# Kernel optimization log

Measured on AMD Instinct MI355X. Metric: run time of the kernel, lower is better.

The kernel has to match this reference:

```python
import jax, jax.numpy as jnp
import numpy as np

B, T, C = 8, 2048, 1024  # micro_bsz, seq_len, n_embd (== complexsize)


def setup_inputs() -> dict:
    key = jax.random.key(0)
    ks = jax.random.split(key, 6)
    w = lambda k, shape: (jax.random.normal(k, shape, dtype=jnp.float32) * 0.02)
    return {
        "x": jax.random.normal(ks[0], (B, T, C), dtype=jnp.float32),
        "Wk": w(ks[1], (2 * C, C)),      # key: n_embd -> 2*n_embd (no bias)
        "Wa": w(ks[2], (C, 2 * C)),      # activation: 2*n_embd -> n_embd (no bias)
        "Wf": w(ks[3], (2, C, C)),       # WaveNet filter conv, kernel=2, WIO layout
        "Wg": w(ks[4], (2, C, C)),       # WaveNet gate conv, kernel=2, WIO layout
        "Wo": w(ks[5], (C, C)),          # WaveNet 1x1 output projection
    }


def _causal_conv(x, W):
    # x: [B,T,Cin], W: [K,Cin,Cout]; left-pad K-1 for causality
    return jax.lax.conv_general_dilated(
        x, W, window_strides=(1,), padding=[(W.shape[0] - 1, 0)],
        dimension_numbers=("NWC", "WIO", "NWC"))


def _wavenet_short(x, Wf, Wg, Wo):
    # undialated gated WaveNet unit: tanh(conv_f(x)) * sigmoid(conv_g(x)) -> 1x1 proj
    h = jnp.tanh(_causal_conv(x, Wf)) * jax.nn.sigmoid(_causal_conv(x, Wg))
    return h @ Wo.T


def reference(x, Wk, Wa, Wf, Wg, Wo):
    Bx, Tx, Cx = x.shape
    k = (x @ Wk.T).reshape(Bx, Tx, Cx, 2)                 # [B,T,C,2]
    cv = jax.lax.complex(k[..., 0], k[..., 1])            # view_as_complex -> [B,T,C]
    scale = jax.lax.cummax(jnp.abs(cv), axis=1)           # running max of magnitude
    cv2 = cv / scale.astype(cv.dtype)                      # normalize magnitude <= 1
    kv = jnp.cumprod(cv2, axis=1)                          # complex cumulative product
    re = jnp.stack([kv.real, kv.imag], axis=-1).reshape(Bx, Tx, 2 * Cx)  # view_as_real
    return (re @ Wa.T) * _wavenet_short(x * scale, Wf, Wg, Wo)
```

## Files before the change

kernel.cpp:

```cpp
#include <hip/hip_runtime.h>
#include <cmath>

#define T_SEQ 2048
#define C_DIM 1024
#define BM 128
#define BN 128
#define BK 32

typedef unsigned short u16;
typedef unsigned int u32;
typedef short bf16x8 __attribute__((ext_vector_type(8)));
typedef _Float16 f16x8 __attribute__((ext_vector_type(8)));
typedef float f32x4 __attribute__((ext_vector_type(4)));
typedef unsigned short u16x8 __attribute__((ext_vector_type(8)));

#define AS1 __attribute__((address_space(1)))
#define AS3 __attribute__((address_space(3)))

__device__ __forceinline__ u16 f2bf(float f) {
    u32 u = __builtin_bit_cast(u32, f);
    u32 r = u + 0x7fffu + ((u >> 16) & 1u);
    return (u16)(r >> 16);
}
__device__ __forceinline__ u16 f2h(float f) {
    return __builtin_bit_cast(u16, (_Float16)f);
}
__device__ __forceinline__ float h2f(u16 h) {
    return (float)__builtin_bit_cast(_Float16, h);
}
__device__ __forceinline__ void gl_lds16(const void* g, void* l) {
    __builtin_amdgcn_global_load_lds((const AS1 u32*)g, (AS3 u32*)l, 16, 0, 0);
}

__device__ __forceinline__ int xcd_swz(int lin, int nwg) {
    return (lin & 7) * (nwg >> 3) + (lin >> 3);
}

#define SBAR() do { __builtin_amdgcn_sched_barrier(0); \
                    __builtin_amdgcn_s_barrier(); \
                    __builtin_amdgcn_sched_barrier(0); } while (0)
#define VMC(n) do { asm volatile("s_waitcnt vmcnt(" #n ")" ::: "memory"); \
                    __builtin_amdgcn_sched_barrier(0); } while (0)

__global__ __launch_bounds__(512, 2)
void gemm8(const u16* __restrict__ Ap, const u16* __restrict__ Bp,
           u16* __restrict__ Cout, int M, int N, int K)
{
    __shared__ u16 lds[2 * 32768];
    const int tid  = threadIdx.x;
    const int lane = tid & 63;
    const int wid  = tid >> 6;
    const int wrow = wid >> 2;
    const int wcol = wid & 3;
    const int gx = gridDim.x;
    const int lin = xcd_swz(blockIdx.x + gx * blockIdx.y, gx * gridDim.y);
    const int m0 = (lin / gx) * 256;
    const int n0 = (lin % gx) * 256;
    const int NT = K / 64;

    f32x4 acc[8][4] = {};

    auto stageu = [&](int t, int u) {
        const int isB = u & 1, kh = u >> 1;
        u16* ubase = &lds[(t & 1) * 32768 + isB * 16384 + kh * 8192];
        const u16* src = isB ? Bp + (size_t)n0 * K : Ap + (size_t)m0 * K;
        const int k0 = t * 64 + kh * 32;
        #pragma unroll
        for (int j = 0; j < 2; ++j) {
            const int c = wid + 8 * j;
            const int p = c * 64 + lane;
            const int row = p >> 2;
            const int sp  = (p & 3) ^ ((row >> 1) & 3);
            gl_lds16(src + (size_t)row * K + k0 + sp * 8, ubase + c * 512);
        }
    };

    auto lda = [&](int buf, int kh, int mq, f16x8 (&a)[4]) {
        const u16* base = &lds[buf * 32768 + kh * 8192];
        #pragma unroll
        for (int f = 0; f < 4; ++f) {
            const int row = wrow * 128 + mq * 64 + f * 16 + (lane & 15);
            const int sp  = (lane >> 4) ^ ((row >> 1) & 3);
            a[f] = *(const f16x8*)&base[row * 32 + sp * 8];
        }
    };
    auto ldb = [&](int buf, int kh, f16x8 (&b)[4]) {
        const u16* base = &lds[buf * 32768 + 16384 + kh * 8192];
        #pragma unroll
        for (int f = 0; f < 4; ++f) {
            const int row = wcol * 64 + f * 16 + (lane & 15);
            const int sp  = (lane >> 4) ^ ((row >> 1) & 3);
            b[f] = *(const f16x8*)&base[row * 32 + sp * 8];
        }
    };
    auto mm = [&](const f16x8 (&a)[4], const f16x8 (&b)[4], int mq) {
        __builtin_amdgcn_s_setprio(1);
        #pragma unroll
        for (int fm = 0; fm < 4; ++fm)
            #pragma unroll
            for (int fn = 0; fn < 4; ++fn)
                acc[mq * 4 + fm][fn] = __builtin_amdgcn_mfma_f32_16x16x32_f16(
                    a[fm], b[fn], acc[mq * 4 + fm][fn], 0, 0, 0);
        __builtin_amdgcn_s_setprio(0);
    };

    stageu(0, 0); stageu(0, 1); stageu(0, 2); stageu(0, 3);
    VMC(4);
    SBAR();

    f16x8 a[4], b[4];
    for (int t = 0; t < NT; ++t) {
        const int buf = t & 1;
        const bool more = (t + 1 < NT);
        if (more) { stageu(t + 1, 0); VMC(6); } else { VMC(4); }
        lda(buf, 0, 0, a); ldb(buf, 0, b);
        mm(a, b, 0);
        SBAR();
        if (more) stageu(t + 1, 1);
        lda(buf, 0, 1, a);
        mm(a, b, 1);
        SBAR();
        if (more) { stageu(t + 1, 2); VMC(6); } else { VMC(0); }
        lda(buf, 1, 0, a); ldb(buf, 1, b);
        mm(a, b, 0);
        SBAR();
        if (more) stageu(t + 1, 3);
        lda(buf, 1, 1, a);
        mm(a, b, 1);
        SBAR();
    }

    const int crow0 = m0 + wrow * 128 + ((lane >> 4) << 2);
    const int ccol  = n0 + wcol * 64 + (lane & 15);
    #pragma unroll
    for (int mi = 0; mi < 8; ++mi)
        #pragma unroll
        for (int fn = 0; fn < 4; ++fn)
            #pragma unroll
            for (int r = 0; r < 4; ++r)
                Cout[(size_t)(crow0 + mi * 16 + r) * N + ccol + fn * 16] =
                    f2h(acc[mi][fn][r]);
}

__global__ __launch_bounds__(256)
void dual_gemm(const u16* __restrict__ A1, const u16* __restrict__ B1, int K1,
               const u16* __restrict__ A2, const u16* __restrict__ B2, int K2,
               float* __restrict__ out, int M, int N)
{
    __shared__ u16 lds[2 * 2 * 4096];
    const int tid  = threadIdx.x;
    const int lane = tid & 63;
    const int wid  = tid >> 6;
    const int wr = wid >> 1, wc = wid & 1;
    const int gx = gridDim.x;
    const int lin = xcd_swz(blockIdx.x + gx * blockIdx.y, gx * gridDim.y);
    const int m0 = (lin / gx) * BM;
    const int n0 = (lin % gx) * BN;

    f32x4 acc1[4][4] = {};
    f32x4 acc2[4][4] = {};

    auto stage = [&](const u16* Ap, const u16* Bp, int K, int it, int buf) {
        const int k0 = it * BK;
        u16* base = &lds[buf * 8192];
        #pragma unroll
        for (int i = 0; i < 2; ++i) {
            const int chunk = wid + 4 * i;
            const int rloc  = chunk * 16 + (lane >> 2);
            const int slot  = (lane & 3) ^ ((rloc >> 1) & 3);
            gl_lds16(Bp + (size_t)(n0 + rloc) * K + k0 + slot * 8,
                     base + 4096 + chunk * 512);
            gl_lds16(Ap + (size_t)(m0 + rloc) * K + k0 + slot * 8,
                     base + chunk * 512);
        }
    };

    auto compute = [&](int buf, f32x4 (&acc)[4][4]) {
        const u16* base = &lds[buf * 8192];
        bf16x8 a[4], b[4];
        #pragma unroll
        for (int f = 0; f < 4; ++f) {
            const int row = wr * 64 + f * 16 + (lane & 15);
            const int sp  = ((lane >> 4) & 3) ^ ((row >> 1) & 3);
            a[f] = *(const bf16x8*)&base[row * 32 + sp * 8];
            const int rowb = wc * 64 + f * 16 + (lane & 15);
            const int spb  = ((lane >> 4) & 3) ^ ((rowb >> 1) & 3);
            b[f] = *(const bf16x8*)&base[4096 + rowb * 32 + spb * 8];
        }
        #pragma unroll
        for (int fm = 0; fm < 4; ++fm)
            #pragma unroll
            for (int fn = 0; fn < 4; ++fn)
                acc[fm][fn] = __builtin_amdgcn_mfma_f32_16x16x32_bf16(a[fm], b[fn], acc[fm][fn], 0, 0, 0);
    };

    const int NT1 = K1 / BK, NT2 = K2 / BK;
    stage(A1, B1, K1, 0, 0);
    int cur = 0;
    for (int it = 0; it < NT1; ++it) {
        __syncthreads();
        if (it + 1 < NT1) stage(A1, B1, K1, it + 1, cur ^ 1);
        else              stage(A2, B2, K2, 0, cur ^ 1);
        compute(cur, acc1);
        cur ^= 1;
    }
    for (int it = 0; it < NT2; ++it) {
        __syncthreads();
        if (it + 1 < NT2) stage(A2, B2, K2, it + 1, cur ^ 1);
        compute(cur, acc2);
        cur ^= 1;
    }

    const int crow0 = m0 + wr * 64 + ((lane >> 4) << 2);
    const int ccol  = n0 + wc * 64 + (lane & 15);
    #pragma unroll
    for (int fm = 0; fm < 4; ++fm)
        #pragma unroll
        for (int fn = 0; fn < 4; ++fn)
            #pragma unroll
            for (int r = 0; r < 4; ++r) {
                const size_t idx = (size_t)(crow0 + fm * 16 + r) * N + ccol + fn * 16;
                out[idx] = acc1[fm][fn][r] * acc2[fm][fn][r];
            }
}

__global__ __launch_bounds__(256)
void conv_gate(const u16* __restrict__ A, const u16* __restrict__ Wfgt,
               u16* __restrict__ H, int M)
{
    constexpr int KIT = C_DIM / BK;
    constexpr int NT  = 2 * KIT;
    __shared__ u16 lds[2 * 3 * 4096];
    const int tid  = threadIdx.x;
    const int lane = tid & 63;
    const int wid  = tid >> 6;
    const int wr = wid >> 1, wc = wid & 1;
    const int gx = gridDim.x;
    const int lin = xcd_swz(blockIdx.x + gx * blockIdx.y, gx * gridDim.y);
    const int m0 = (lin / gx) * BM;
    const int n0 = (lin % gx) * BN;

    f32x4 accF[4][4] = {};
    f32x4 accG[4][4] = {};

    auto stage = [&](int it, int buf) {
        const int p  = it / KIT;
        const int k0 = (it - p * KIT) * BK;
        u16* base = &lds[buf * 12288];
        const u16* BF = Wfgt + (size_t)p * 2 * C_DIM * C_DIM;
        const u16* BG = BF + (size_t)C_DIM * C_DIM;
        const int sh = (p == 0) ? 1 : 0;
        #pragma unroll
        for (int i = 0; i < 2; ++i) {
            const int chunk = wid + 4 * i;
            const int rloc  = chunk * 16 + (lane >> 2);
            const int slot  = (lane & 3) ^ ((rloc >> 1) & 3);
            int grow = m0 + rloc - sh;
            if (grow < 0) grow = 0;
            gl_lds16(A + (size_t)grow * C_DIM + k0 + slot * 8,
                     base + chunk * 512);
            gl_lds16(BF + (size_t)(n0 + rloc) * C_DIM + k0 + slot * 8,
                     base + 4096 + chunk * 512);
            gl_lds16(BG + (size_t)(n0 + rloc) * C_DIM + k0 + slot * 8,
                     base + 8192 + chunk * 512);
        }
    };

    auto compute = [&](int buf) {
        const u16* base = &lds[buf * 12288];
        bf16x8 a[4], bf[4], bg[4];
        #pragma unroll
        for (int f = 0; f < 4; ++f) {
            const int row = wr * 64 + f * 16 + (lane & 15);
            const int sp  = ((lane >> 4) & 3) ^ ((row >> 1) & 3);
            a[f] = *(const bf16x8*)&base[row * 32 + sp * 8];
            const int rowb = wc * 64 + f * 16 + (lane & 15);
            const int spb  = ((lane >> 4) & 3) ^ ((rowb >> 1) & 3);
            bf[f] = *(const bf16x8*)&base[4096 + rowb * 32 + spb * 8];
            bg[f] = *(const bf16x8*)&base[8192 + rowb * 32 + spb * 8];
        }
        #pragma unroll
        for (int fm = 0; fm < 4; ++fm)
            #pragma unroll
            for (int fn = 0; fn < 4; ++fn) {
                accF[fm][fn] = __builtin_amdgcn_mfma_f32_16x16x32_bf16(a[fm], bf[fn], accF[fm][fn], 0, 0, 0);
                accG[fm][fn] = __builtin_amdgcn_mfma_f32_16x16x32_bf16(a[fm], bg[fn], accG[fm][fn], 0, 0, 0);
            }
    };

    stage(0, 0);
    int cur = 0;
    for (int it = 0; it < NT; ++it) {
        __syncthreads();
        if ((it / KIT) == 0 && (m0 % T_SEQ) == 0) {
            if (tid < 4) {
                u16x8 z = {0,0,0,0,0,0,0,0};
                *(u16x8*)&lds[cur * 12288 + tid * 8] = z;
            }
            __syncthreads();
        }
        if (it + 1 < NT) stage(it + 1, cur ^ 1);
        compute(cur);
        cur ^= 1;
    }

    const int crow0 = m0 + wr * 64 + ((lane >> 4) << 2);
    const int ccol  = n0 + wc * 64 + (lane & 15);
    #pragma unroll
    for (int fm = 0; fm < 4; ++fm)
        #pragma unroll
        for (int fn = 0; fn < 4; ++fn)
            #pragma unroll
            for (int r = 0; r < 4; ++r) {
                const float fv = accF[fm][fn][r];
                const float gv = accG[fm][fn][r];
                const float th = 1.0f - 2.0f / (expf(2.0f * fv) + 1.0f);
                const float sg = 1.0f / (1.0f + expf(-gv));
                H[(size_t)(crow0 + fm * 16 + r) * C_DIM + ccol + fn * 16] = f2bf(th * sg);
            }
}

#define SSEG 32
#define SCHB 32
#define SSL (T_SEQ / SSEG)

__global__ __launch_bounds__(1024, 1)
void scan_kernel(u16* __restrict__ kq, u16* __restrict__ xyb)
{
    __shared__ float  lmax[SSEG][SCHB];
    __shared__ float2 lprod[SSEG][SCHB];
    const int blk = blockIdx.x;
    const int b   = blk >> 5;
    const int c0  = (blk & 31) * SCHB;
    const int ch  = threadIdx.x & (SCHB - 1);
    const int seg = threadIdx.x >> 5;
    const int c   = c0 + ch;
    const int t0  = seg * SSL;
    const size_t baseh = (size_t)b * T_SEQ * 2048 + 2 * c + (size_t)t0 * 2048;
    const size_t base1 = (size_t)b * T_SEQ * C_DIM + c + (size_t)t0 * C_DIM;

    float m2 = 0.f;
    {
        size_t idx = baseh;
        for (int t = 0; t < SSL; ++t) {
            const u32 v = *(const u32*)&kq[idx];
            const float re = h2f((u16)(v & 0xffffu));
            const float im = h2f((u16)(v >> 16));
            m2 = fmaxf(m2, re * re + im * im);
            idx += 2048;
        }
    }
    lmax[seg][ch] = sqrtf(m2);
    __syncthreads();
    #pragma unroll
    for (int s = 1; s < SSEG; s <<= 1) {
        const float v = lmax[seg][ch];
        const float u = (seg >= s) ? lmax[seg - s][ch] : 0.f;
        __syncthreads();
        lmax[seg][ch] = fmaxf(v, u);
        __syncthreads();
    }
    const float premax = (seg > 0) ? lmax[seg - 1][ch] : 0.f;

    float pr = 1.f, pi = 0.f;
    float m = premax;
    {
        size_t idx = baseh, idx1 = base1;
        for (int t = 0; t < SSL; ++t) {
            const u32 v = *(const u32*)&kq[idx];
            const float re = h2f((u16)(v & 0xffffu));
            const float im = h2f((u16)(v >> 16));
            m = fmaxf(m, sqrtf(re * re + im * im));
            const float inv = 1.f / m;
            const float r0 = re * inv, r1 = im * inv;
            const float nr = pr * r0 - pi * r1;
            const float ni = pr * r1 + pi * r0;
            pr = nr; pi = ni;
            const float xv = h2f(xyb[idx1]);
            xyb[idx1] = f2bf(xv * m);
            idx += 2048; idx1 += C_DIM;
        }
    }
    lprod[seg][ch] = make_float2(pr, pi);
    __syncthreads();
    #pragma unroll
    for (int s = 1; s < SSEG; s <<= 1) {
        const float2 v = lprod[seg][ch];
        const float2 u = (seg >= s) ? lprod[seg - s][ch] : make_float2(1.f, 0.f);
        __syncthreads();
        lprod[seg][ch] = make_float2(u.x * v.x - u.y * v.y,
                                     u.x * v.y + u.y * v.x);
        __syncthreads();
    }
    float ppr = 1.f, ppi = 0.f;
    if (seg > 0) { const float2 pp = lprod[seg - 1][ch]; ppr = pp.x; ppi = pp.y; }

    pr = 1.f; pi = 0.f;
    m = premax;
    {
        size_t idx = baseh;
        for (int t = 0; t < SSL; ++t) {
            const u32 v = *(const u32*)&kq[idx];
            const float re = h2f((u16)(v & 0xffffu));
            const float im = h2f((u16)(v >> 16));
            m = fmaxf(m, sqrtf(re * re + im * im));
            const float inv = 1.f / m;
            const float r0 = re * inv, r1 = im * inv;
            const float nr = pr * r0 - pi * r1;
            const float ni = pr * r1 + pi * r0;
            pr = nr; pi = ni;
            const float fr = ppr * nr - ppi * ni;
            const float fi = ppr * ni + ppi * nr;
            *(u32*)&kq[idx] = ((u32)f2bf(fi) << 16) | (u32)f2bf(fr);
            idx += 2048;
        }
    }
}

__global__ void cvt_weights(const float* __restrict__ Wk, const float* __restrict__ Wa,
                            const float* __restrict__ Wo, u16* __restrict__ Wkh,
                            u16* __restrict__ Wab, u16* __restrict__ Wob)
{
    const int n1 = 2048 * 1024, n2 = 2 * 2048 * 1024, n3 = n2 + 1024 * 1024;
    const int i = (blockIdx.x * blockDim.x + threadIdx.x) * 4;
    if (i < n1) {
        const float4 v = *(const float4*)&Wk[i];
        ushort4 o; o.x = f2h(v.x); o.y = f2h(v.y); o.z = f2h(v.z); o.w = f2h(v.w);
        *(ushort4*)&Wkh[i] = o;
    } else if (i < n2) {
        const int j = i - n1;
        const float4 v = *(const float4*)&Wa[j];
        ushort4 o; o.x = f2bf(v.x); o.y = f2bf(v.y); o.z = f2bf(v.z); o.w = f2bf(v.w);
        *(ushort4*)&Wab[j] = o;
    } else if (i < n3) {
        const int j = i - n2;
        const float4 v = *(const float4*)&Wo[j];
        ushort4 o; o.x = f2bf(v.x); o.y = f2bf(v.y); o.z = f2bf(v.z); o.w = f2bf(v.w);
        *(ushort4*)&Wob[j] = o;
    }
}

__global__ void cvt_f16(const float* __restrict__ src, u16* __restrict__ dst, int n)
{
    const int i = (blockIdx.x * blockDim.x + threadIdx.x) * 4;
    if (i >= n) return;
    const float4 v = *(const float4*)&src[i];
    ushort4 o;
    o.x = f2h(v.x); o.y = f2h(v.y); o.z = f2h(v.z); o.w = f2h(v.w);
    *(ushort4*)&dst[i] = o;
}

__global__ __launch_bounds__(256)
void wtrans(const float* __restrict__ Wf, const float* __restrict__ Wg,
            u16* __restrict__ dst)
{
    __shared__ float tile[64][65];
    const int z = blockIdx.z;
    const float* src = ((z < 2) ? Wf : Wg) + (size_t)(z & 1) * C_DIM * C_DIM;
    u16* d = dst + (size_t)(z & 1) * (2 * C_DIM) * C_DIM
                 + ((z < 2) ? (size_t)0 : (size_t)C_DIM * C_DIM);
    const int k0 = blockIdx.x * 64;
    const int n0 = blockIdx.y * 64;
    const int tx = threadIdx.x & 63, ty = threadIdx.x >> 6;
    #pragma unroll
    for (int i = 0; i < 16; ++i) {
        const int r = ty + i * 4;
        tile[r][tx] = src[(size_t)(k0 + r) * C_DIM + n0 + tx];
    }
    __syncthreads();
    #pragma unroll
    for (int i = 0; i < 16; ++i) {
        const int r = ty + i * 4;
        d[(size_t)(n0 + r) * C_DIM + k0 + tx] = f2bf(tile[tx][r]);
    }
}

extern "C" void kernel_launch(void* const* d_in, const int* in_sizes, int n_in,
                              void* d_out, int out_size, void* d_ws, size_t ws_size,
                              hipStream_t stream)
{
    const float* x  = (const float*)d_in[0];
    const float* Wk = (const float*)d_in[1];
    const float* Wa = (const float*)d_in[2];
    const float* Wf = (const float*)d_in[3];
    const float* Wg = (const float*)d_in[4];
    const float* Wo = (const float*)d_in[5];
    float* out = (float*)d_out;

    const int M = 8 * T_SEQ;
    u16* kq   = (u16*)d_ws;
    u16* yb   = (u16*)((char*)d_ws + 67108864ull);
    u16* hb   = (u16*)((char*)d_ws + 100663296ull);
    u16* Wkh  = (u16*)((char*)d_ws + 134217728ull);
    u16* Wab  = Wkh + 2048 * 1024;
    u16* Wfgt = Wab + 2048 * 1024;
    u16* Wob  = Wfgt + 2ull * 2048 * 1024;

    cvt_weights<<<(5 * 1024 * 1024 / 4 + 255) / 256, 256, 0, stream>>>(
        Wk, Wa, Wo, Wkh, Wab, Wob);
    wtrans  <<<dim3(16, 16, 4), 256, 0, stream>>>(Wf, Wg, Wfgt);
    cvt_f16 <<<(M * 1024 / 4) / 256, 256, 0, stream>>>(x, yb, M * 1024);

    gemm8<<<dim3(2048 / 256, M / 256), 512, 0, stream>>>(
        yb, Wkh, kq, M, 2048, 1024);

    scan_kernel<<<256, 1024, 0, stream>>>(kq, yb);

    conv_gate<<<dim3(1024 / BN, M / BM), 256, 0, stream>>>(yb, Wfgt, hb, M);

    dual_gemm<<<dim3(1024 / BN, M / BM), 256, 0, stream>>>(
        kq, Wab, 2048, hb, Wob, 1024, out, M, 1024);
}
```

Before: 454.9 us.

## Replace conv_gate with 8-wave 256x128 pipelined conv kernel

The gated causal conv kernel is rewritten to use 512-thread blocks with a 256x128 output tile (filter and gate each 128 wide), BK=64 split into two 32-wide halves. It issues global-to-LDS loads for A and B in stages that interleave with MFMA work, using explicit vmcnt waits, raw barriers and setprio around the MFMA bursts. The aim is to raise MFMA utilisation and hide load latency compared with the simple double-buffered 128x128 kernel. In exchange it needs more LDS and registers per block, and the hand-tuned wait counts are fragile.

```diff
diff --git a/kernel.cpp b/kernel.cpp
--- a/kernel.cpp
+++ b/kernel.cpp
@@ -142,6 +142,146 @@
                     f2h(acc[mi][fn][r]);
 }
 
+__global__ __launch_bounds__(512, 2)
+void conv8(const u16* __restrict__ A, const u16* __restrict__ Wfgt,
+           u16* __restrict__ H, int M)
+{
+    __shared__ u16 lds[2 * 32768];
+    const int tid  = threadIdx.x;
+    const int lane = tid & 63;
+    const int wid  = tid >> 6;
+    const int wrow = wid >> 2;
+    const int wcol = wid & 3;
+    const int gx = gridDim.x;
+    const int lin = xcd_swz(blockIdx.x + gx * blockIdx.y, gx * gridDim.y);
+    const int m0 = (lin / gx) * 256;
+    const int n0 = (lin % gx) * 128;
+    const int NT = 32;
+
+    f32x4 accF[8][2] = {};
+    f32x4 accG[8][2] = {};
+
+    auto stageA = [&](int t, int kh) {
+        u16* ubase = &lds[(t & 1) * 32768 + kh * 8192];
+        const int tap = t >> 4;
+        const int k0 = (t & 15) * 64 + kh * 32;
+        const int sh = (tap == 0) ? 1 : 0;
+        #pragma unroll
+        for (int j = 0; j < 2; ++j) {
+            const int c = wid + 8 * j;
+            const int p = c * 64 + lane;
+            const int row = p >> 2;
+            const int sp  = (p & 3) ^ ((row >> 1) & 3);
+            int grow = m0 + row - sh;
+            if (grow < 0) grow = 0;
+            gl_lds16(A + (size_t)grow * C_DIM + k0 + sp * 8, ubase + c * 512);
+        }
+    };
+    auto stageB = [&](int t, int kh) {
+        u16* ubase = &lds[(t & 1) * 32768 + 16384 + kh * 8192];
+        const int tap = t >> 4;
+        const int k0 = (t & 15) * 64 + kh * 32;
+        const u16* BF = Wfgt + (size_t)tap * 2 * C_DIM * C_DIM;
+        const u16* BG = BF + (size_t)C_DIM * C_DIM;
+        #pragma unroll
+        for (int j = 0; j < 2; ++j) {
+            const int c = wid + 8 * j;
+            const int isG = c >> 3;
+            const int p = (c & 7) * 64 + lane;
+            const int row = p >> 2;
+            const int sp  = (p & 3) ^ ((row >> 1) & 3);
+            const u16* src = (isG ? BG : BF) + (size_t)(n0 + row) * C_DIM + k0 + sp * 8;
+            gl_lds16(src, ubase + isG * 4096 + (c & 7) * 512);
+        }
+    };
+
+    auto lda8 = [&](int buf, int kh, bf16x8 (&a)[8]) {
+        const u16* base = &lds[buf * 32768 + kh * 8192];
+        #pragma unroll
+        for (int f = 0; f < 8; ++f) {
+            const int row = wrow * 128 + f * 16 + (lane & 15);
+            const int sp  = (lane >> 4) ^ ((row >> 1) & 3);
+            a[f] = *(const bf16x8*)&base[row * 32 + sp * 8];
+        }
+    };
+    auto ldb2 = [&](int buf, int kh, int isG, bf16x8 (&b)[2]) {
+        const u16* base = &lds[buf * 32768 + 16384 + kh * 8192 + isG * 4096];
+        #pragma unroll
+        for (int f = 0; f < 2; ++f) {
+            const int row = wcol * 32 + f * 16 + (lane & 15);
+            const int sp  = (lane >> 4) ^ ((row >> 1) & 3);
+            b[f] = *(const bf16x8*)&base[row * 32 + sp * 8];
+        }
+    };
+    auto mm2 = [&](const bf16x8 (&a)[8], const bf16x8 (&b)[2], f32x4 (&acc)[8][2]) {
+        __builtin_amdgcn_s_setprio(1);
+        #pragma unroll
+        for (int fm = 0; fm < 8; ++fm)
+            #pragma unroll
+            for (int fn = 0; fn < 2; ++fn)
+                acc[fm][fn] = __builtin_amdgcn_mfma_f32_16x16x32_bf16(
+                    a[fm], b[fn], acc[fm][fn], 0, 0, 0);
+        __builtin_amdgcn_s_setprio(0);
+    };
+
+    const bool zrow = (m0 % T_SEQ) == 0;
+
+    auto zeroA = [&](int buf, int kh) {
+        if (tid < 4) {
+            u16x8 zz = {0,0,0,0,0,0,0,0};
+            *(u16x8*)&lds[buf * 32768 + kh * 8192 + tid * 8] = zz;
+        }
+        asm volatile("s_waitcnt lgkmcnt(0)" ::: "memory");
+        __builtin_amdgcn_sched_barrier(0);
+        __builtin_amdgcn_s_barrier();
+        __builtin_amdgcn_sched_barrier(0);
+    };
+
+    stageA(0, 0); stageB(0, 0); stageA(0, 1); stageB(0, 1);
+    VMC(4);
+    SBAR();
+
+    bf16x8 a[8], bF[2], bG[2];
+    for (int t = 0; t < NT; ++t) {
+        const int buf = t & 1;
+        const bool more = (t + 1 < NT);
+        const bool z0 = zrow && (t < 16);
+        if (more) { stageA(t + 1, 0); VMC(6); } else { VMC(4); }
+        if (z0) zeroA(buf, 0);
+        lda8(buf, 0, a); ldb2(buf, 0, 0, bF);
+        mm2(a, bF, accF);
+        SBAR();
+        if (more) stageB(t + 1, 0);
+        ldb2(buf, 0, 1, bG);
+        mm2(a, bG, accG);
+        SBAR();
+        if (more) { stageA(t + 1, 1); VMC(6); } else { VMC(0); }
+        if (z0) zeroA(buf, 1);
+        lda8(buf, 1, a); ldb2(buf, 1, 0, bF);
+        mm2(a, bF, accF);
+        SBAR();
+        if (more) stageB(t + 1, 1);
+        ldb2(buf, 1, 1, bG);
+        mm2(a, bG, accG);
+        SBAR();
+    }
+
+    const int crow0 = m0 + wrow * 128 + ((lane >> 4) << 2);
+    const int ccol  = n0 + wcol * 32 + (lane & 15);
+    #pragma unroll
+    for (int fm = 0; fm < 8; ++fm)
+        #pragma unroll
+        for (int fn = 0; fn < 2; ++fn)
+            #pragma unroll
+            for (int r = 0; r < 4; ++r) {
+                const float fv = accF[fm][fn][r];
+                const float gv = accG[fm][fn][r];
+                const float th = 1.0f - 2.0f / (expf(2.0f * fv) + 1.0f);
+                const float sg = 1.0f / (1.0f + expf(-gv));
+                H[(size_t)(crow0 + fm * 16 + r) * C_DIM + ccol + fn * 16] = f2bf(th * sg);
+            }
+}
+
 __global__ __launch_bounds__(256)
 void dual_gemm(const u16* __restrict__ A1, const u16* __restrict__ B1, int K1,
                const u16* __restrict__ A2, const u16* __restrict__ B2, int K2,
@@ -221,102 +361,6 @@
             for (int r = 0; r < 4; ++r) {
                 const size_t idx = (size_t)(crow0 + fm * 16 + r) * N + ccol + fn * 16;
                 out[idx] = acc1[fm][fn][r] * acc2[fm][fn][r];
-            }
-}
-
-__global__ __launch_bounds__(256)
-void conv_gate(const u16* __restrict__ A, const u16* __restrict__ Wfgt,
-               u16* __restrict__ H, int M)
-{
-    constexpr int KIT = C_DIM / BK;
-    constexpr int NT  = 2 * KIT;
-    __shared__ u16 lds[2 * 3 * 4096];
-    const int tid  = threadIdx.x;
-    const int lane = tid & 63;
-    const int wid  = tid >> 6;
-    const int wr = wid >> 1, wc = wid & 1;
-    const int gx = gridDim.x;
-    const int lin = xcd_swz(blockIdx.x + gx * blockIdx.y, gx * gridDim.y);
-    const int m0 = (lin / gx) * BM;
-    const int n0 = (lin % gx) * BN;
-
-    f32x4 accF[4][4] = {};
-    f32x4 accG[4][4] = {};
-
-    auto stage = [&](int it, int buf) {
-        const int p  = it / KIT;
-        const int k0 = (it - p * KIT) * BK;
-        u16* base = &lds[buf * 12288];
-        const u16* BF = Wfgt + (size_t)p * 2 * C_DIM * C_DIM;
-        const u16* BG = BF + (size_t)C_DIM * C_DIM;
-        const int sh = (p == 0) ? 1 : 0;
-        #pragma unroll
-        for (int i = 0; i < 2; ++i) {
-            const int chunk = wid + 4 * i;
-            const int rloc  = chunk * 16 + (lane >> 2);
-            const int slot  = (lane & 3) ^ ((rloc >> 1) & 3);
-            int grow = m0 + rloc - sh;
-            if (grow < 0) grow = 0;
-            gl_lds16(A + (size_t)grow * C_DIM + k0 + slot * 8,
-                     base + chunk * 512);
-            gl_lds16(BF + (size_t)(n0 + rloc) * C_DIM + k0 + slot * 8,
-                     base + 4096 + chunk * 512);
-            gl_lds16(BG + (size_t)(n0 + rloc) * C_DIM + k0 + slot * 8,
-                     base + 8192 + chunk * 512);
-        }
-    };
-
-    auto compute = [&](int buf) {
-        const u16* base = &lds[buf * 12288];
-        bf16x8 a[4], bf[4], bg[4];
-        #pragma unroll
-        for (int f = 0; f < 4; ++f) {
-            const int row = wr * 64 + f * 16 + (lane & 15);
-            const int sp  = ((lane >> 4) & 3) ^ ((row >> 1) & 3);
-            a[f] = *(const bf16x8*)&base[row * 32 + sp * 8];
-            const int rowb = wc * 64 + f * 16 + (lane & 15);
-            const int spb  = ((lane >> 4) & 3) ^ ((rowb >> 1) & 3);
-            bf[f] = *(const bf16x8*)&base[4096 + rowb * 32 + spb * 8];
-            bg[f] = *(const bf16x8*)&base[8192 + rowb * 32 + spb * 8];
-        }
-        #pragma unroll
-        for (int fm = 0; fm < 4; ++fm)
-            #pragma unroll
-            for (int fn = 0; fn < 4; ++fn) {
-                accF[fm][fn] = __builtin_amdgcn_mfma_f32_16x16x32_bf16(a[fm], bf[fn], accF[fm][fn], 0, 0, 0);
-                accG[fm][fn] = __builtin_amdgcn_mfma_f32_16x16x32_bf16(a[fm], bg[fn], accG[fm][fn], 0, 0, 0);
-            }
-    };
-
-    stage(0, 0);
-    int cur = 0;
-    for (int it = 0; it < NT; ++it) {
-        __syncthreads();
-        if ((it / KIT) == 0 && (m0 % T_SEQ) == 0) {
-            if (tid < 4) {
-                u16x8 z = {0,0,0,0,0,0,0,0};
-                *(u16x8*)&lds[cur * 12288 + tid * 8] = z;
-            }
-            __syncthreads();
-        }
-        if (it + 1 < NT) stage(it + 1, cur ^ 1);
-        compute(cur);
-        cur ^= 1;
-    }
-
-    const int crow0 = m0 + wr * 64 + ((lane >> 4) << 2);
-    const int ccol  = n0 + wc * 64 + (lane & 15);
-    #pragma unroll
-    for (int fm = 0; fm < 4; ++fm)
-        #pragma unroll
-        for (int fn = 0; fn < 4; ++fn)
-            #pragma unroll
-            for (int r = 0; r < 4; ++r) {
-                const float fv = accF[fm][fn][r];
-                const float gv = accG[fm][fn][r];
-                const float th = 1.0f - 2.0f / (expf(2.0f * fv) + 1.0f);
-                const float sg = 1.0f / (1.0f + expf(-gv));
-                H[(size_t)(crow0 + fm * 16 + r) * C_DIM + ccol + fn * 16] = f2bf(th * sg);
             }
 }
 
@@ -506,7 +550,7 @@
 
     scan_kernel<<<256, 1024, 0, stream>>>(kq, yb);
 
-    conv_gate<<<dim3(1024 / BN, M / BM), 256, 0, stream>>>(yb, Wfgt, hb, M);
+    conv8<<<dim3(1024 / 128, M / 256), 512, 0, stream>>>(yb, Wfgt, hb, M);
 
     dual_gemm<<<dim3(1024 / BN, M / BM), 256, 0, stream>>>(
         kq, Wab, 2048, hb, Wob, 1024, out, M, 1024);
```

Measured after the change: 450.3 us. No clear change (-1.0%).
